# Kernel optimization log

Hardware: AMD Instinct MI355X
Metric: run time of the kernel (lower is better)

Reference implementation:

```python
import jax, jax.numpy as jnp
import numpy as np

# BatchNorm1d in eval mode with default init (gamma=1, beta=0, mean=0, var=1):
# y = x / sqrt(1 + eps)
BN_S = 1.0 / float(np.sqrt(1.0 + 1e-5))
ROI_THRESH = 0.8
DN = ('NCHW', 'OIHW', 'NCHW')


def conv(x, w, stride=1, pad=1):
    return jax.lax.conv_general_dilated(x, w, (stride, stride), ((pad, pad), (pad, pad)), dimension_numbers=DN)


def inv_conv(x, w):
    # dense equivalent of spconv.SparseInverseConv2d paired with a stride-2, pad-1, k=3 conv:
    # adjoint index map = transposed conv (lhs_dilation=2, flipped kernel, pad (1,2))
    return jax.lax.conv_general_dilated(x, jnp.flip(w, (2, 3)), (1, 1), ((1, 2), (1, 2)), lhs_dilation=(2, 2), dimension_numbers=DN)


def downsample_mask(m):
    # active-site generation rule of a stride-2, pad-1, k=3 sparse conv == 3x3/stride-2 max pool
    return jax.lax.reduce_window(m, 0.0, jax.lax.max, (1, 1, 3, 3), (1, 1, 2, 2), ((0, 0), (0, 0), (1, 1), (1, 1)))


def setup_inputs():
    key = jax.random.key(0)
    ks = jax.random.split(key, 24)
    b, n_i, H, W = 2, 4, 384, 384
    s = 0.1  # weight scale to keep activations bounded through the conv stack
    inp = {
        'x': jax.random.normal(ks[0], (b, 64, H // 4, W // 4), jnp.float32),
        'image': jax.random.normal(ks[1], (b, 3, H, W), jnp.float32),
        'masks': jax.random.uniform(ks[2], (b, n_i, H, W), jnp.float32),
        'roi_masks': jax.random.uniform(ks[3], (b, n_i, H, W), jnp.float32),
        'w1a': jax.random.normal(ks[4], (32, 4, 3, 3), jnp.float32) * s,
        'w1b': jax.random.normal(ks[5], (32, 32, 3, 3), jnp.float32) * s,
        'w2a': jax.random.normal(ks[6], (32, 32, 3, 3), jnp.float32) * s,
        'w2b': jax.random.normal(ks[7], (32, 32, 3, 3), jnp.float32) * s,
        'w4a': jax.random.normal(ks[8], (64, 32, 3, 3), jnp.float32) * s,
        'w4b': jax.random.normal(ks[9], (64, 64, 3, 3), jnp.float32) * s,
        'inv4_w': jax.random.normal(ks[10], (64, 64, 3, 3), jnp.float32) * s,
        'l4_sub_w': jax.random.normal(ks[11], (32, 64, 3, 3), jnp.float32) * s,
        'inv2_w': jax.random.normal(ks[12], (32, 32, 3, 3), jnp.float32) * s,
        'l5_sub_w': jax.random.normal(ks[13], (32, 32, 3, 3), jnp.float32) * s,
        'r4_w1': jax.random.normal(ks[14], (32, 64, 3, 3), jnp.float32) * s,
        'r4_w2': jax.random.normal(ks[15], (1, 32, 3, 3), jnp.float32) * s,
        'r4_b2': jax.random.normal(ks[16], (1,), jnp.float32) * s,
        'r1_w1': jax.random.normal(ks[17], (32, 32, 3, 3), jnp.float32) * s,
        'r1_w2': jax.random.normal(ks[18], (1, 32, 3, 3), jnp.float32) * s,
        'r1_b2': jax.random.normal(ks[19], (1,), jnp.float32) * s,
    }
    return inp


def reference(x, image, masks, roi_masks, w1a, w1b, w2a, w2b, w4a, w4b, inv4_w, l4_sub_w, inv2_w, l5_sub_w, r4_w1, r4_w2, r4_b2, r1_w1, r1_w2, r1_b2):
    # Faithful dense emulation of predict_details: SubMConv == conv(masked x)*mask,
    # stride-2 SparseConv == conv(masked x) masked by max-pooled mask,
    # SparseInverseConv == transposed conv masked by parent-resolution mask,
    # Fsp.sparse_add on shared indices == masked add, dense()-99/+99 == where(mask, v, -99).
    b, n_i, H, W = masks.shape
    N = b * n_i
    m = masks.reshape(N, 1, H, W)
    roi = roi_masks.reshape(N, 1, H, W)
    img = jnp.broadcast_to(image[:, None], (b, n_i, 3, H, W)).reshape(N, 3, H, W)
    inp = jnp.concatenate([img, m], axis=1)  # [N,4,H,W]

    mask1 = (roi > ROI_THRESH).astype(inp.dtype)
    mask2 = downsample_mask(mask1)
    mask4 = downsample_mask(mask2)

    # low_os1_module: SubMConv, ReLU, BN, SubMConv, ReLU, BN
    f = jnp.maximum(conv(inp * mask1, w1a) * mask1, 0.0) * BN_S
    fea1 = jnp.maximum(conv(f, w1b) * mask1, 0.0) * BN_S  # [N,32,H,W]
    # low_os2_module: stride-2 SparseConv, ReLU, BN, SubMConv, ReLU, BN
    g = jnp.maximum(conv(fea1, w2a, stride=2) * mask2, 0.0) * BN_S
    fea2 = jnp.maximum(conv(g, w2b) * mask2, 0.0) * BN_S  # [N,32,H/2,W/2]
    # low_os4_module
    h = jnp.maximum(conv(fea2, w4a, stride=2) * mask4, 0.0) * BN_S
    fea3 = jnp.maximum(conv(h, w4b) * mask4, 0.0) * BN_S  # [N,64,H/4,W/4]

    # gather dense OS4 features at sparse sites (batch index // n_i) + sparse_add
    xg = jnp.broadcast_to(x[:, None], (b, n_i) + x.shape[1:]).reshape(N, *x.shape[1:]) * mask4
    xs = xg + fea3

    # refine_OS4: SubMConv, BN, leaky, SubMConv(+bias); dense() with -99 off-support
    t = jax.nn.leaky_relu(conv(xs, r4_w1) * mask4 * BN_S, 0.2)
    t = (conv(t, r4_w2) + r4_b2[None, :, None, None]) * mask4
    x_os4_out = jnp.where(mask4 > 0, t, -99.0)

    # layer4: SparseInverseConv(64->64) to OS2 sites, BN, leaky, SubMConv(64->32); add fea2
    u = jax.nn.leaky_relu(inv_conv(xs, inv4_w) * mask2 * BN_S, 0.2)
    u = conv(u, l4_sub_w) * mask2 + fea2
    # layer5: SparseInverseConv(32->32) to OS1 sites, BN, leaky, SubMConv(32->32); add fea1
    v = jax.nn.leaky_relu(inv_conv(u, inv2_w) * mask1 * BN_S, 0.2)
    v = conv(v, l5_sub_w) * mask1 + fea1

    # refine_OS1
    t1 = jax.nn.leaky_relu(conv(v, r1_w1) * mask1 * BN_S, 0.2)
    t1 = (conv(t1, r1_w2) + r1_b2[None, :, None, None]) * mask1
    x_os1_out = jnp.where(mask1 > 0, t1, -99.0)
    return x_os4_out, x_os1_out
```

## Files before the change

kernel.cpp:

```cpp
#include <hip/hip_runtime.h>
#include <hip/hip_bf16.h>

using bf16 = __hip_bfloat16;
typedef unsigned char u8;
typedef short bf16x8 __attribute__((ext_vector_type(8)));
typedef short bf16x4 __attribute__((ext_vector_type(4)));
typedef float f32x4 __attribute__((ext_vector_type(4)));

#define BNS 0.9999950000374997f
#define MFMA_B16 __builtin_amdgcn_mfma_f32_16x16x32_bf16

__device__ __forceinline__ short f2bs(float v){ bf16 h = __float2bfloat16(v); return *reinterpret_cast<short*>(&h); }
__device__ __forceinline__ float s2f(short s){ union{unsigned u; float f;} x; x.u = ((unsigned)(unsigned short)s) << 16; return x.f; }
__device__ __forceinline__ float lrelu(float a){ return fmaxf(a, 0.2f*a); }
__device__ __forceinline__ bf16x8 ld8(const short* p){ return *(const bf16x8*)(p); }

__global__ __launch_bounds__(256) void k_prep(const float* __restrict__ roi,
                                              const float* __restrict__ w1b,
                                              const float* __restrict__ i2,
                                              const float* __restrict__ l5,
                                              const float* __restrict__ r1a,
                                              const float* __restrict__ w2b,
                                              const float* __restrict__ w2a,
                                              const float* __restrict__ inv4,
                                              const float* __restrict__ w4b,
                                              const float* __restrict__ l4s,
                                              const float* __restrict__ r4w1,
                                              const float* __restrict__ w4a,
                                              const float* __restrict__ w1a,
                                              const float* __restrict__ r1w2,
                                              const float* __restrict__ r4w2,
                                              u8* __restrict__ M1, u8* __restrict__ M2, u8* __restrict__ M4,
                                              short* __restrict__ WT, short* __restrict__ WT4,
                                              short* __restrict__ d1a, short* __restrict__ dh)
{
    const int HW1 = 384*384, HW2 = 192*192, HW4 = 96*96;
    int bid = blockIdx.x, tid = threadIdx.x;
    if (bid < 4608){
        int i = bid*256 + tid;
        M1[i] = (roi[i] > 0.8f) ? 1 : 0;
    } else if (bid < 5760){
        int i = (bid-4608)*256 + tid;
        int n = i / HW2, p = i - n*HW2;
        int oy = p / 192, ox = p - oy*192;
        const float* r = roi + (size_t)n*HW1;
        int v = 0;
        #pragma unroll
        for (int ky=0; ky<3; ky++){
            int iy = 2*oy + ky - 1;
            if ((unsigned)iy >= 384u) continue;
            #pragma unroll
            for (int kx=0; kx<3; kx++){
                int ix = 2*ox + kx - 1;
                if ((unsigned)ix < 384u) v |= (r[iy*384 + ix] > 0.8f);
            }
        }
        M2[i] = (u8)v;
    } else if (bid < 6048){
        int i = (bid-5760)*256 + tid;
        int n = i / HW4, p = i - n*HW4;
        int oy = p / 96, ox = p - oy*96;
        const float* r = roi + (size_t)n*HW1;
        int v = 0;
        for (int dy=-3; dy<=3; dy++){
            int iy = 4*oy + dy;
            if ((unsigned)iy >= 384u) continue;
            for (int dx=-3; dx<=3; dx++){
                int ix = 4*ox + dx;
                if ((unsigned)ix < 384u) v |= (r[iy*384 + ix] > 0.8f);
            }
        }
        M4[i] = (u8)v;
    } else if (bid < 6264){
        int local = bid - 6048;
        int a = local / 36;
        int j = (local - a*36)*256 + tid;
        const float* src = (a==0)? w1b : (a==1)? i2 : (a==2)? l5 : (a==3)? r1a : (a==4)? w2b : w2a;
        float sc = (a==2) ? 1.0f : BNS;
        if (j < 9216){
            int co = j/288, r = j%288, ci = r/9, k = r%9;
            WT[a*9216 + k*1024 + co*32 + ci] = f2bs(src[j]*sc);
        }
    } else if (bid < 6984){
        int local = bid - 6264;
        int a = local / 144;
        int j = (local - a*144)*256 + tid;
        if (a < 2){
            if (j < 36864){
                int co = j/576, r = j%576, ci = r/9, k = r%9;
                const float* s = a ? w4b : inv4;
                WT4[a*36864 + k*4096 + co*64 + ci] = f2bs(s[j]*BNS);
            }
        } else if (a < 4){
            if (j < 18432){
                int co = j/576, r = j%576, ci = r/9, k = r%9;
                const float* s = (a==2) ? l4s : r4w1;
                float sc = (a==2) ? 1.0f : BNS;
                WT4[73728 + (a-2)*18432 + k*2048 + co*64 + ci] = f2bs(s[j]*sc);
            }
        } else {
            if (j < 18432){
                int co = j/288, r = j%288, ci = r/9, k = r%9;
                WT4[110592 + k*2048 + co*32 + ci] = f2bs(w4a[j]*BNS);
            }
        }
    } else {
        int local = bid - 6984;
        int a = local / 18;
        int j = (local - a*18)*256 + tid;
        if (a == 0){
            if (j < 2048){
                int h = j >> 10, r = j & 1023, co = r >> 5, kq = r & 31;
                int q = h*32 + kq;
                d1a[j] = (q < 36) ? f2bs(w1a[co*36 + q]*BNS) : 0;
            }
        } else {
            if (j < 4608){
                int k = j/512, r = j%512, co = r/32, ci = r%32;
                const float* s = (a==1) ? r1w2 : r4w2;
                dh[(a-1)*4608 + j] = (co == 0) ? f2bs(s[ci*9 + k]) : 0;
            }
        }
    }
}

template<int CIN, int COUT, int EPI, int TH>
__global__ __launch_bounds__(256) void mconv_s1(const short* __restrict__ in, int H,
                                                const short* __restrict__ wT,
                                                const u8* __restrict__ mask,
                                                const float* __restrict__ res32,
                                                short* __restrict__ out, int tilesX)
{
    const int HW = H*H;
    const int HV = CIN/32, G = COUT/16, CH8 = CIN/8;
    const int SR = TH + 2;
    const int SITES = SR*18;
    const int PS = (SITES | 1)*8;
    const int U2N = TH/4;
    int tY = blockIdx.x / tilesX, tX = blockIdx.x % tilesX, n = blockIdx.z;
    int y0 = tY*TH, x0 = tX*16;

    __shared__ __align__(16) short s_in[CH8*((SITES|1)*8)];
    __shared__ u8 s_m[TH*16];

    int tid = threadIdx.x;
    const short* inN = in + (size_t)n*HW*CIN;
    for (int i = tid; i < SITES*CH8; i += 256){
        int r = i/CH8, q = i%CH8;
        int ry = r/18, rx = r%18;
        int gy = y0-1+ry, gx = x0-1+rx;
        bf16x8 v = {0,0,0,0,0,0,0,0};
        if ((unsigned)gy < (unsigned)H && (unsigned)gx < (unsigned)H)
            v = *(const bf16x8*)(inN + ((size_t)gy*H + gx)*CIN + q*8);
        *(bf16x8*)(s_in + q*PS + r*8) = v;
    }
    for (int i = tid; i < TH*16; i += 256){
        int ty = i>>4, tx = i&15;
        s_m[i] = mask[(size_t)n*HW + (y0+ty)*H + x0+tx];
    }
    __syncthreads();

    int wv = tid >> 6, lane = tid & 63;
    int nQ = lane >> 4, nn = lane & 15;

    f32x4 acc[U2N][G];
    #pragma unroll
    for (int u2=0; u2<U2N; ++u2)
        #pragma unroll
        for (int g=0; g<G; ++g) acc[u2][g] = (f32x4){0,0,0,0};

    #pragma unroll
    for (int h=0; h<HV; ++h){
        const short* bh[U2N];
        #pragma unroll
        for (int u2=0; u2<U2N; ++u2){
            int ty = u2*4 + wv;
            bh[u2] = s_in + (h*4+nQ)*PS + (ty*18 + nn)*8;
        }
        #pragma unroll
        for (int ky=0; ky<3; ++ky)
            #pragma unroll
            for (int kx=0; kx<3; ++kx){
                const int k = ky*3+kx;
                bf16x8 a[G];
                #pragma unroll
                for (int g=0; g<G; ++g)
                    a[g] = *(const bf16x8*)(wT + k*COUT*CIN + (g*16+nn)*CIN + h*32 + nQ*8);
                #pragma unroll
                for (int u2=0; u2<U2N; ++u2){
                    bf16x8 bfr = ld8(bh[u2] + (ky*18+kx)*8);
                    #pragma unroll
                    for (int g=0; g<G; ++g)
                        acc[u2][g] = MFMA_B16(a[g], bfr, acc[u2][g], 0,0,0);
                }
            }
    }

    #pragma unroll
    for (int u2=0; u2<U2N; ++u2){
        int nt = u2*4 + wv;
        int p = (y0+nt)*H + x0+nn;
        u8 m = s_m[nt*16 + nn];
        short* op = out + ((size_t)n*HW + p)*COUT;
        #pragma unroll
        for (int g=0; g<G; ++g){
            float r[4];
            #pragma unroll
            for (int e=0; e<4; ++e){
                int co = g*16 + nQ*4 + e;
                float a = acc[u2][g][e], o;
                if      (EPI == 0) o = m ? fmaxf(a,0.f) : 0.f;
                else if (EPI == 1) o = m ? lrelu(a) : 0.f;
                else o = m ? fmaxf(a,0.f) + res32[((size_t)(n>>2)*COUT + co)*(size_t)HW + p] : 0.f;
                r[e] = o;
            }
            bf16x4 w4 = {f2bs(r[0]),f2bs(r[1]),f2bs(r[2]),f2bs(r[3])};
            *(bf16x4*)(op + g*16 + nQ*4) = w4;
        }
    }
}

template<int COUT, int THO>
__global__ __launch_bounds__(256) void mconv_s2m(const short* __restrict__ in, int IH,
                                                 const short* __restrict__ wT,
                                                 const u8* __restrict__ mask,
                                                 short* __restrict__ out, int OH, int tilesX)
{
    const int IHW = IH*IH, OHW = OH*OH, G = COUT/16;
    const int IR = 2*THO + 1;
    const int SITES = IR*33;
    const int PS = (SITES|1)*8;
    const int ITN = THO/4;
    int tY = blockIdx.x / tilesX, tX = blockIdx.x % tilesX, n = blockIdx.z;
    int y0 = tY*THO, x0 = tX*16;

    __shared__ __align__(16) short s_in[4*((SITES|1)*8)];
    __shared__ u8 s_m[THO*16];

    int tid = threadIdx.x;
    const short* inN = in + (size_t)n*IHW*32;
    for (int i = tid; i < SITES*4; i += 256){
        int r = i>>2, q = i&3;
        int ry = r/33, rx = r%33;
        int gy = 2*y0-1+ry, gx = 2*x0-1+rx;
        bf16x8 v = {0,0,0,0,0,0,0,0};
        if ((unsigned)gy < (unsigned)IH && (unsigned)gx < (unsigned)IH)
            v = *(const bf16x8*)(inN + ((size_t)gy*IH + gx)*32 + q*8);
        *(bf16x8*)(s_in + q*PS + r*8) = v;
    }
    for (int i = tid; i < THO*16; i += 256){
        int ty = i>>4, tx = i&15;
        s_m[i] = mask[(size_t)n*OHW + (y0+ty)*OH + x0+tx];
    }
    __syncthreads();

    int wv = tid >> 6, lane = tid & 63;
    int nQ = lane >> 4, nn = lane & 15;

    f32x4 acc[ITN][G];
    #pragma unroll
    for (int it=0; it<ITN; ++it)
        #pragma unroll
        for (int g=0; g<G; ++g) acc[it][g] = (f32x4){0,0,0,0};

    const short* pb[ITN];
    #pragma unroll
    for (int it=0; it<ITN; ++it){
        int nt = it*4 + wv;
        pb[it] = s_in + nQ*PS + ((2*nt)*33 + 2*nn)*8;
    }

    #pragma unroll
    for (int ky=0; ky<3; ++ky)
        #pragma unroll
        for (int kx=0; kx<3; ++kx){
            const int k = ky*3+kx;
            bf16x8 a[G];
            #pragma unroll
            for (int g=0; g<G; ++g)
                a[g] = *(const bf16x8*)(wT + k*COUT*32 + (g*16+nn)*32 + nQ*8);
            #pragma unroll
            for (int it=0; it<ITN; ++it){
                bf16x8 bfr = ld8(pb[it] + (ky*33+kx)*8);
                #pragma unroll
                for (int g=0; g<G; ++g)
                    acc[it][g] = MFMA_B16(a[g], bfr, acc[it][g], 0,0,0);
            }
        }

    #pragma unroll
    for (int it=0; it<ITN; ++it){
        int nt = it*4 + wv;
        int p = (y0+nt)*OH + x0+nn;
        u8 m = s_m[nt*16 + nn];
        short* op = out + ((size_t)n*OHW + p)*COUT;
        #pragma unroll
        for (int g=0; g<G; ++g){
            float r[4];
            #pragma unroll
            for (int e=0; e<4; ++e) r[e] = m ? fmaxf(acc[it][g][e],0.f) : 0.f;
            bf16x4 w4 = {f2bs(r[0]),f2bs(r[1]),f2bs(r[2]),f2bs(r[3])};
            *(bf16x4*)(op + g*16 + nQ*4) = w4;
        }
    }
}

template<int TH>
__global__ __launch_bounds__(256) void mconv_ref4(const short* __restrict__ in, int H,
                                                  const short* __restrict__ wTa,
                                                  const short* __restrict__ wTh,
                                                  const float* __restrict__ bias,
                                                  const u8* __restrict__ mask,
                                                  float* __restrict__ out, int tilesX)
{
    const int HW = H*H;
    const int XR = TH+4, XSITES = XR*20;
    const int PSX = (XSITES|1)*8;
    const int TR = TH+2, TSITES = TR*18;
    const int PST = (TSITES|1)*8;
    int tY = blockIdx.x / tilesX, tX = blockIdx.x % tilesX, n = blockIdx.z;
    int y0 = tY*TH, x0 = tX*16;

    __shared__ __align__(16) short s_xs[8*((XSITES|1)*8)];
    __shared__ __align__(16) short s_t[4*((TSITES|1)*8)];
    __shared__ u8 s_m[TSITES];

    int tid = threadIdx.x;
    const short* inN = in + (size_t)n*HW*64;
    for (int i = tid; i < XSITES*8; i += 256){
        int r = i>>3, q = i&7;
        int ry = r/20, rx = r%20;
        int gy = y0-2+ry, gx = x0-2+rx;
        bf16x8 v = {0,0,0,0,0,0,0,0};
        if ((unsigned)gy < (unsigned)H && (unsigned)gx < (unsigned)H)
            v = *(const bf16x8*)(inN + ((size_t)gy*H + gx)*64 + q*8);
        *(bf16x8*)(s_xs + q*PSX + r*8) = v;
    }
    for (int i = tid; i < TSITES; i += 256){
        int vy = i/18, vx = i%18;
        int gy = y0-1+vy, gx = x0-1+vx;
        s_m[i] = ((unsigned)gy < (unsigned)H && (unsigned)gx < (unsigned)H) ? mask[(size_t)n*HW + gy*H + gx] : 0;
    }
    __syncthreads();

    int wv = tid >> 6, lane = tid & 63;
    int nQ = lane >> 4, nn = lane & 15;

    const int TG = (TSITES + 15)/16;
    for (int g8 = wv; g8 < TG; g8 += 4){
        int s0 = g8*16 + nn;
        int s = s0 >= TSITES ? TSITES-1 : s0;
        int vy = s/18, vx = s - vy*18;
        const short* pb = s_xs + nQ*PSX + (vy*20 + vx)*8;
        f32x4 acc0 = {0,0,0,0}, acc1 = {0,0,0,0};
        #pragma unroll
        for (int ky=0; ky<3; ++ky)
            #pragma unroll
            for (int kx=0; kx<3; ++kx){
                const int k = ky*3+kx;
                const short* wk = wTa + k*2048;
                bf16x8 xlo = ld8(pb + (ky*20+kx)*8);
                bf16x8 xhi = ld8(pb + 4*PSX + (ky*20+kx)*8);
                bf16x8 a0lo = *(const bf16x8*)(wk + nn*64 + nQ*8);
                bf16x8 a0hi = *(const bf16x8*)(wk + nn*64 + 32 + nQ*8);
                bf16x8 a1lo = *(const bf16x8*)(wk + (16+nn)*64 + nQ*8);
                bf16x8 a1hi = *(const bf16x8*)(wk + (16+nn)*64 + 32 + nQ*8);
                acc0 = MFMA_B16(a0lo, xlo, acc0, 0,0,0);
                acc0 = MFMA_B16(a0hi, xhi, acc0, 0,0,0);
                acc1 = MFMA_B16(a1lo, xlo, acc1, 0,0,0);
                acc1 = MFMA_B16(a1hi, xhi, acc1, 0,0,0);
            }
        if (s0 < TSITES){
            u8 m = s_m[s0];
            #pragma unroll
            for (int g=0; g<2; ++g){
                float r[4];
                #pragma unroll
                for (int e=0; e<4; ++e){
                    float a = g ? acc1[e] : acc0[e];
                    r[e] = m ? lrelu(a) : 0.f;
                }
                bf16x4 w4 = {f2bs(r[0]),f2bs(r[1]),f2bs(r[2]),f2bs(r[3])};
                *(bf16x4*)(s_t + (g*2 + (nQ>>1))*PST + s0*8 + (nQ&1)*4) = w4;
            }
        }
    }
    __syncthreads();

    float bb = bias[0];
    for (int nt = wv; nt < TH; nt += 4){
        const short* pt = s_t + nQ*PST + (nt*18 + nn)*8;
        f32x4 acc = {0,0,0,0};
        #pragma unroll
        for (int ky=0; ky<3; ++ky)
            #pragma unroll
            for (int kx=0; kx<3; ++kx){
                const int k = ky*3+kx;
                bf16x8 aw = *(const bf16x8*)(wTh + k*512 + nn*32 + nQ*8);
                bf16x8 bfr = ld8(pt + (ky*18+kx)*8);
                acc = MFMA_B16(aw, bfr, acc, 0,0,0);
            }
        if (nQ == 0){
            u8 m = s_m[(nt+1)*18 + nn+1];
            out[(size_t)n*HW + (size_t)(y0+nt)*H + (x0+nn)] = m ? acc[0] + bb : -99.f;
        }
    }
}

__global__ __launch_bounds__(256) void conv1ab3(const float* __restrict__ image,
                                                const float* __restrict__ masks,
                                                const u8*  __restrict__ M1,
                                                const short* __restrict__ wT1a,
                                                const short* __restrict__ wT1b,
                                                short* __restrict__ fea1)
{
    const int H = 384; const int HW = H*H;
    const int PS = 181*8;
    int tY = blockIdx.x / 48, tX = blockIdx.x % 48, n = blockIdx.z;
    int y0 = tY*16, x0 = tX*8;

    __shared__ float s_inp[4][240];
    __shared__ u8    s_m[240];
    __shared__ int   s_cnt[2];
    __shared__ unsigned short s_lF[180];
    __shared__ unsigned short s_lO[128];
    __shared__ __align__(16) short s_ic[8*(181*8)];
    __shared__ __align__(16) short s_f[4*(181*8)];

    int tid = threadIdx.x;
    const bf16x8 Z8 = {0,0,0,0,0,0,0,0};
    if (tid < 2) s_cnt[tid] = 0;
    for (int i = tid; i < 4*181; i += 256)
        *(bf16x8*)(s_f + i*8) = Z8;
    for (int i = tid; i < 240; i += 256){
        int ly = i/12, lxx = i%12;
        int gy = y0-2+ly, gx = x0-2+lxx;
        bool inb = ((unsigned)gy < 384u) && ((unsigned)gx < 384u);
        u8 mv = inb ? M1[(size_t)n*HW + gy*H + gx] : 0;
        s_m[i] = mv;
        float mm = (float)mv;
        int p = gy*H + gx;
        #pragma unroll
        for (int c = 0; c < 4; ++c){
            float v = 0.f;
            if (inb) v = (c < 3) ? image[((size_t)(n>>2)*3 + c)*HW + p]
                                 : masks[(size_t)n*HW + p];
            s_inp[c][i] = v*mm;
        }
    }
    __syncthreads();

    for (int i = tid; i < 180; i += 256){
        int fy = i/10, fx = i - fy*10;
        if (s_m[(fy+1)*12 + fx+1]){
            int idx = atomicAdd(&s_cnt[0], 1);
            s_lF[idx] = (unsigned short)i;
        }
    }
    for (int i = tid; i < 128; i += 256){
        int ty = i>>3, tx = i&7;
        if (s_m[(ty+2)*12 + tx+2]){
            int idx = atomicAdd(&s_cnt[1], 1);
            s_lO[idx] = (unsigned short)i;
        }
    }
    __syncthreads();

    int cntF = s_cnt[0], cntO = s_cnt[1];

    {
        int q = tid & 63;
        int ci = q/9, kk = q - ci*9, ky = kk/3, kx = kk - ky*3;
        bool qok = q < 36;
        for (int i = tid; i < cntF*64; i += 256){
            int site = s_lF[i >> 6];
            short v = 0;
            if (qok){
                int fy = site/10, fx = site - fy*10;
                v = f2bs(s_inp[ci][(fy+ky)*12 + fx+kx]);
            }
            s_ic[(q>>3)*PS + site*8 + (q&7)] = v;
        }
    }
    __syncthreads();

    int wv = tid >> 6, lane = tid & 63;
    int nQ = lane >> 4, nn = lane & 15;

    {
        bf16x8 fa0[2], fa1[2];
        #pragma unroll
        for (int h=0;h<2;++h){
            fa0[h] = *(const bf16x8*)(wT1a + h*1024 + nn*32 + nQ*8);
            fa1[h] = *(const bf16x8*)(wT1a + h*1024 + (16+nn)*32 + nQ*8);
        }
        for (int base = wv*16; base < cntF; base += 64){
            int slot = base + nn;
            bool on = slot < cntF;
            int site = s_lF[on ? slot : 0];
            f32x4 a0 = {0,0,0,0}, a1 = {0,0,0,0};
            #pragma unroll
            for (int h=0;h<2;++h){
                bf16x8 bfr = ld8(s_ic + (h*4+nQ)*PS + site*8);
                a0 = MFMA_B16(fa0[h], bfr, a0, 0,0,0);
                a1 = MFMA_B16(fa1[h], bfr, a1, 0,0,0);
            }
            if (on){
                #pragma unroll
                for (int g=0; g<2; ++g){
                    float r[4];
                    #pragma unroll
                    for (int e=0; e<4; ++e){
                        float a = g ? a1[e] : a0[e];
                        r[e] = fmaxf(a,0.f);
                    }
                    bf16x4 w4 = {f2bs(r[0]),f2bs(r[1]),f2bs(r[2]),f2bs(r[3])};
                    *(bf16x4*)(s_f + (g*2 + (nQ>>1))*PS + site*8 + (nQ&1)*4) = w4;
                }
            }
        }
    }
    __syncthreads();

    {
        for (int base = wv*16; base < cntO; base += 64){
            int slot = base + nn;
            bool on = slot < cntO;
            int os = s_lO[on ? slot : 0];
            int ty = os >> 3, tx = os & 7;
            const short* pb = s_f + nQ*PS + (ty*10 + tx)*8;
            f32x4 acc0 = {0,0,0,0}, acc1 = {0,0,0,0};
            #pragma unroll
            for (int ky=0; ky<3; ++ky)
                #pragma unroll
                for (int kx=0; kx<3; ++kx){
                    const int k = ky*3+kx;
                    bf16x8 a0 = *(const bf16x8*)(wT1b + k*1024 + nn*32 + nQ*8);
                    bf16x8 a1 = *(const bf16x8*)(wT1b + k*1024 + (16+nn)*32 + nQ*8);
                    bf16x8 bfr = ld8(pb + (ky*10+kx)*8);
                    acc0 = MFMA_B16(a0, bfr, acc0, 0,0,0);
                    acc1 = MFMA_B16(a1, bfr, acc1, 0,0,0);
                }
            if (on){
                short* fp = fea1 + ((size_t)n*HW + (size_t)(y0+ty)*H + (x0+tx))*32;
                #pragma unroll
                for (int g=0; g<2; ++g){
                    float r[4];
                    #pragma unroll
                    for (int e=0; e<4; ++e){
                        float a = g ? acc1[e] : acc0[e];
                        r[e] = fmaxf(a,0.f);
                    }
                    bf16x4 w4 = {f2bs(r[0]),f2bs(r[1]),f2bs(r[2]),f2bs(r[3])};
                    *(bf16x4*)(fp + g*16 + nQ*4) = w4;
                }
            }
        }
        for (int i = tid; i < 128*4; i += 256){
            int os = i >> 2, q = i & 3;
            int ty = os >> 3, tx = os & 7;
            if (!s_m[(ty+2)*12 + tx+2])
                *(bf16x8*)(fea1 + ((size_t)n*HW + (size_t)(y0+ty)*H + (x0+tx))*32 + q*8) = Z8;
        }
    }
}

__global__ __launch_bounds__(256) void fk_l4c(const short* __restrict__ xs,
                                              const short* __restrict__ fea2,
                                              const u8*  __restrict__ M2,
                                              const short* __restrict__ wTi4,
                                              const short* __restrict__ wTl4,
                                              short* __restrict__ u_out)
{
    const int H2 = 192, HW2 = H2*H2, H4 = 96, HW4 = H4*H4;
    const int PSX = 101*8, PSU = 325*8;
    int tY = blockIdx.x / 12, tX = blockIdx.x % 12, n = blockIdx.z;
    int y0 = tY*16, x0 = tX*16;
    int uy0 = (y0>>1) - 1, ux0 = (x0>>1) - 1;

    __shared__ __align__(16) short s_xs[8*(101*8)];
    __shared__ __align__(16) short s_ul[8*(325*8)];
    __shared__ u8 s_m[324];

    int tid = threadIdx.x;
    const short* xN = xs + (size_t)n*HW4*64;
    for (int i = tid; i < 100*8; i += 256){
        int r = i>>3, q = i&7;
        int ly = r/10, lxx = r%10;
        int gy = uy0+ly, gx = ux0+lxx;
        bf16x8 v = {0,0,0,0,0,0,0,0};
        if ((unsigned)gy < 96u && (unsigned)gx < 96u)
            v = *(const bf16x8*)(xN + ((size_t)gy*H4 + gx)*64 + q*8);
        *(bf16x8*)(s_xs + q*PSX + r*8) = v;
    }
    for (int i = tid; i < 324; i += 256){
        int ry = i/18, rx = i%18; int gy = y0-1+ry, gx = x0-1+rx;
        s_m[i] = ((unsigned)gy < 192u && (unsigned)gx < 192u) ? M2[(size_t)n*HW2 + gy*H2 + gx] : 0;
    }

    int wv = tid >> 6, lane = tid & 63;
    int nQ = lane >> 4, nn = lane & 15;

    bf16x4 pf2v[4][2];
    {
        const short* f2N = fea2 + (size_t)n*HW2*32;
        #pragma unroll
        for (int u2=0; u2<4; ++u2){
            int nt = u2*4 + wv;
            int p = (y0+nt)*H2 + x0+nn;
            const short* fp = f2N + (size_t)p*32;
            pf2v[u2][0] = *(const bf16x4*)(fp + nQ*4);
            pf2v[u2][1] = *(const bf16x4*)(fp + 16 + nQ*4);
        }
    }
    __syncthreads();

    for (int ui = wv; ui < 24; ui += 4){
        int cls = ui/6, nt = ui%6;
        int pY = cls >> 1, pX = cls & 1;
        int s0 = nt*16 + nn;
        int s = s0 > 80 ? 80 : s0;
        int jr = s/9, jc = s%9;
        int ry = 2*jr + pY, rx = 2*jc + pX;

        int tiy[4], tix[4], twk[4]; int tapN;
        if (pY == 0){
            if (pX == 0){
                tiy[0]=jr;   tix[0]=jc;   twk[0]=8;
                tiy[1]=jr;   tix[1]=jc+1; twk[1]=6;
                tiy[2]=jr+1; tix[2]=jc;   twk[2]=2;
                tiy[3]=jr+1; tix[3]=jc+1; twk[3]=0; tapN=4;
            } else {
                tiy[0]=jr;   tix[0]=jc+1; twk[0]=7;
                tiy[1]=jr+1; tix[1]=jc+1; twk[1]=1; tapN=2;
            }
        } else {
            if (pX == 0){
                tiy[0]=jr+1; tix[0]=jc;   twk[0]=5;
                tiy[1]=jr+1; tix[1]=jc+1; twk[1]=3; tapN=2;
            } else {
                tiy[0]=jr+1; tix[0]=jc+1; twk[0]=4; tapN=1;
            }
        }

        f32x4 acc[4];
        #pragma unroll
        for (int g=0; g<4; ++g) acc[g] = (f32x4){0,0,0,0};
        for (int t = 0; t < tapN; ++t){
            int off = (tiy[t]*10 + tix[t])*8;
            bf16x8 xlo = ld8(s_xs + nQ*PSX + off);
            bf16x8 xhi = ld8(s_xs + (4+nQ)*PSX + off);
            const short* wk = wTi4 + twk[t]*4096;
            #pragma unroll
            for (int g=0; g<4; ++g){
                bf16x8 alo = *(const bf16x8*)(wk + (g*16+nn)*64 + nQ*8);
                bf16x8 ahi = *(const bf16x8*)(wk + (g*16+nn)*64 + 32 + nQ*8);
                acc[g] = MFMA_B16(alo, xlo, acc[g], 0,0,0);
                acc[g] = MFMA_B16(ahi, xhi, acc[g], 0,0,0);
            }
        }
        if (s0 <= 80){
            int sidx = ry*18 + rx;
            u8 m = s_m[sidx];
            #pragma unroll
            for (int g=0; g<4; ++g){
                float r[4];
                #pragma unroll
                for (int e=0; e<4; ++e){
                    float a = acc[g][e];
                    r[e] = m ? lrelu(a) : 0.f;
                }
                bf16x4 w4 = {f2bs(r[0]),f2bs(r[1]),f2bs(r[2]),f2bs(r[3])};
                *(bf16x4*)(s_ul + ((g>>1)*4 + (g&1)*2 + (nQ>>1))*PSU + sidx*8 + (nQ&1)*4) = w4;
            }
        }
    }
    __syncthreads();

    {
        f32x4 acc0[4], acc1[4];
        const short* pv[4];
        #pragma unroll
        for (int u2=0; u2<4; ++u2){
            acc0[u2] = (f32x4){0,0,0,0}; acc1[u2] = (f32x4){0,0,0,0};
            int nt = u2*4 + wv;
            pv[u2] = s_ul + nQ*PSU + (nt*18 + nn)*8;
        }
        #pragma unroll
        for (int ky=0; ky<3; ++ky)
            #pragma unroll
            for (int kx=0; kx<3; ++kx){
                int k = ky*3+kx;
                const short* wk = wTl4 + k*2048;
                bf16x8 a0lo = *(const bf16x8*)(wk + nn*64 + nQ*8);
                bf16x8 a0hi = *(const bf16x8*)(wk + nn*64 + 32 + nQ*8);
                bf16x8 a1lo = *(const bf16x8*)(wk + (16+nn)*64 + nQ*8);
                bf16x8 a1hi = *(const bf16x8*)(wk + (16+nn)*64 + 32 + nQ*8);
                #pragma unroll
                for (int u2=0; u2<4; ++u2){
                    bf16x8 vlo = ld8(pv[u2] + (ky*18+kx)*8);
                    bf16x8 vhi = ld8(pv[u2] + 4*PSU + (ky*18+kx)*8);
                    acc0[u2] = MFMA_B16(a0lo, vlo, acc0[u2], 0,0,0);
                    acc0[u2] = MFMA_B16(a0hi, vhi, acc0[u2], 0,0,0);
                    acc1[u2] = MFMA_B16(a1lo, vlo, acc1[u2], 0,0,0);
                    acc1[u2] = MFMA_B16(a1hi, vhi, acc1[u2], 0,0,0);
                }
            }
        #pragma unroll
        for (int u2 = 0; u2 < 4; ++u2){
            int nt = u2*4 + wv;
            int p = (y0+nt)*H2 + x0+nn;
            u8 m = s_m[(nt+1)*18 + nn+1];
            short* up = u_out + ((size_t)n*HW2 + p)*32;
            #pragma unroll
            for (int g=0; g<2; ++g){
                float r[4];
                #pragma unroll
                for (int e=0; e<4; ++e){
                    float a = g ? acc1[u2][e] : acc0[u2][e];
                    r[e] = m ? a + s2f(pf2v[u2][g][e]) : 0.f;
                }
                bf16x4 w4 = {f2bs(r[0]),f2bs(r[1]),f2bs(r[2]),f2bs(r[3])};
                *(bf16x4*)(up + g*16 + nQ*4) = w4;
            }
        }
    }
}

__global__ __launch_bounds__(256) void fk_back8(const short* __restrict__ u,
                                                const short* __restrict__ fea1,
                                                const u8*  __restrict__ M1,
                                                const short* __restrict__ wTi2,
                                                const short* __restrict__ wTl5,
                                                const short* __restrict__ wTr1a,
                                                const short* __restrict__ wTr1b,
                                                const float* __restrict__ r1_b2,
                                                float* __restrict__ out1)
{
    const int H1 = 384, HW1 = H1*H1, H2 = 192, HW2 = H2*H2;
    const int PS_U = 97*8, PS_A = 309*8, PS_B = 241*8, PS_C = 181*8;
    int tY = blockIdx.x / 48, tX = blockIdx.x % 48, n = blockIdx.z;
    int y0 = tY*16, x0 = tX*8;
    int uy0 = (y0>>1) - 2, ux0 = (x0>>1) - 2;

    __shared__ __align__(16) short sP0[4*(309*8)];
    __shared__ __align__(16) short sP1[4*(241*8)];
    __shared__ u8 s_m[308];
    __shared__ int s_cnt[7];
    __shared__ unsigned s_lA[4*80];
    __shared__ unsigned s_lB[240];
    __shared__ unsigned s_lC[180];
    __shared__ unsigned s_lD[128];
    short* s_u  = sP1;
    short* s_vl = sP0;
    short* s_v  = sP1;
    short* s_t1 = sP0;

    int tid = threadIdx.x;
    const bf16x8 Z8 = {0,0,0,0,0,0,0,0};

    if (tid < 7) s_cnt[tid] = 0;
    const short* uN = u + (size_t)n*HW2*32;
    for (int i = tid; i < 96*4; i += 256){
        int r = i>>2, q = i&3;
        int ly = r >> 3, lxx = r & 7;
        int gy = uy0+ly, gx = ux0+lxx;
        bf16x8 v = Z8;
        if ((unsigned)gy < 192u && (unsigned)gx < 192u)
            v = *(const bf16x8*)(uN + ((size_t)gy*H2 + gx)*32 + q*8);
        *(bf16x8*)(s_u + q*PS_U + r*8) = v;
    }
    for (int i = tid; i < 308; i += 256){
        int ry = i/14, rx = i%14; int gy = y0-3+ry, gx = x0-3+rx;
        s_m[i] = ((unsigned)gy < 384u && (unsigned)gx < 384u) ? M1[(size_t)n*HW1 + gy*H1 + gx] : 0;
    }
    for (int i = tid; i < 4*309; i += 256)
        *(bf16x8*)(s_vl + i*8) = Z8;
    __syncthreads();

    for (int i = tid; i < 308; i += 256){
        if (s_m[i]){
            int ry = i/14, rx = i - ry*14;
            int cls = ((ry&1)<<1) | (rx&1);
            int jr = ry>>1, jc = rx>>1;
            int idx = atomicAdd(&s_cnt[cls], 1);
            s_lA[cls*80 + idx] = ((unsigned)i<<16) | (unsigned)(jr*8+jc);
        }
    }
    for (int i = tid; i < 240; i += 256){
        int vy = i/12, vx = i - vy*12;
        if (s_m[(vy+1)*14 + vx+1]){
            int idx = atomicAdd(&s_cnt[4], 1);
            s_lB[idx] = ((unsigned)i<<16) | (unsigned)(vy*14+vx);
        }
    }
    for (int i = tid; i < 180; i += 256){
        int qy = i/10, qx = i - qy*10;
        if (s_m[(qy+2)*14 + qx+2]){
            int idx = atomicAdd(&s_cnt[5], 1);
            s_lC[idx] = ((unsigned)i<<16) | (unsigned)(qy*12+qx);
        }
    }
    for (int i = tid; i < 128; i += 256){
        int ty = i>>3, tx = i&7;
        if (s_m[(ty+3)*14 + tx+3]){
            int idx = atomicAdd(&s_cnt[6], 1);
            s_lD[idx] = ((unsigned)i<<16) | (unsigned)(ty*10+tx);
        } else {
            out1[(size_t)n*HW1 + (size_t)(y0+ty)*H1 + (x0+tx)] = -99.f;
        }
    }
    __syncthreads();

    int wv = tid >> 6, lane = tid & 63;
    int nQ = lane >> 4, nn = lane & 15;

    int cntB = s_cnt[4];
    bf16x4 pfB[4][2];
    #pragma unroll
    for (int it=0; it<4; ++it){
        int slot = wv*16 + it*64 + nn;
        if (slot < cntB){
            unsigned e = s_lB[slot];
            int wr = e >> 16;
            int vy = wr/12, vx = wr - vy*12;
            const short* f1 = fea1 + ((size_t)n*HW1 + (size_t)(y0-2+vy)*H1 + (x0-2+vx))*32;
            pfB[it][0] = *(const bf16x4*)(f1 + nQ*4);
            pfB[it][1] = *(const bf16x4*)(f1 + 16 + nQ*4);
        }
    }

    {
        const int tN_[4]   = {4,2,2,1};
        const int tOff[4][4] = {{0,1,8,9},{1,9,9,9},{8,9,9,9},{9,9,9,9}};
        const int tWk [4][4] = {{8,6,2,0},{7,1,1,1},{5,3,3,3},{4,4,4,4}};
        int cnt = s_cnt[wv];
        int tn = tN_[wv];
        for (int base = 0; base < cnt; base += 16){
            int slot = base + nn;
            bool on = slot < cnt;
            unsigned e = s_lA[wv*80 + (on ? slot : 0)];
            int rb = e & 0xffff;
            f32x4 acc0 = {0,0,0,0}, acc1 = {0,0,0,0};
            for (int t = 0; t < tn; ++t){
                bf16x8 bfr = ld8(s_u + nQ*PS_U + (rb + tOff[wv][t])*8);
                const short* wp = wTi2 + tWk[wv][t]*1024;
                bf16x8 a0 = *(const bf16x8*)(wp + nn*32 + nQ*8);
                bf16x8 a1 = *(const bf16x8*)(wp + (16+nn)*32 + nQ*8);
                acc0 = MFMA_B16(a0, bfr, acc0, 0,0,0);
                acc1 = MFMA_B16(a1, bfr, acc1, 0,0,0);
            }
            if (on){
                int sidx = e >> 16;
                float r[8];
                #pragma unroll
                for (int g=0; g<2; ++g)
                    #pragma unroll
                    for (int ee=0; ee<4; ++ee)
                        r[g*4+ee] = lrelu(g ? acc1[ee] : acc0[ee]);
                bf16x4 w0 = {f2bs(r[0]),f2bs(r[1]),f2bs(r[2]),f2bs(r[3])};
                bf16x4 w1 = {f2bs(r[4]),f2bs(r[5]),f2bs(r[6]),f2bs(r[7])};
                *(bf16x4*)(s_vl + (nQ>>1)*PS_A     + sidx*8 + (nQ&1)*4) = w0;
                *(bf16x4*)(s_vl + (2+(nQ>>1))*PS_A + sidx*8 + (nQ&1)*4) = w1;
            }
        }
    }
    __syncthreads();

    for (int i = tid; i < 4*241; i += 256)
        *(bf16x8*)(s_v + i*8) = Z8;
    __syncthreads();

    {
        #pragma unroll
        for (int it=0; it<4; ++it){
            int base = wv*16 + it*64;
            if (base < cntB){
                int slot = base + nn;
                bool on = slot < cntB;
                unsigned e = s_lB[on ? slot : 0];
                int rb = e & 0xffff;
                int wr = e >> 16;
                const short* pv = s_vl + nQ*PS_A + rb*8;
                f32x4 acc0 = {0,0,0,0}, acc1 = {0,0,0,0};
                #pragma unroll
                for (int ky=0; ky<3; ++ky)
                    #pragma unroll
                    for (int kx=0; kx<3; ++kx){
                        const int k = ky*3+kx;
                        bf16x8 wb0 = *(const bf16x8*)(wTl5 + k*1024 + nn*32 + nQ*8);
                        bf16x8 wb1 = *(const bf16x8*)(wTl5 + k*1024 + (16+nn)*32 + nQ*8);
                        bf16x8 bfr = ld8(pv + (ky*14+kx)*8);
                        acc0 = MFMA_B16(wb0, bfr, acc0, 0,0,0);
                        acc1 = MFMA_B16(wb1, bfr, acc1, 0,0,0);
                    }
                if (on){
                    float r[8];
                    #pragma unroll
                    for (int ee=0; ee<4; ++ee){
                        r[ee]   = acc0[ee] + s2f(pfB[it][0][ee]);
                        r[4+ee] = acc1[ee] + s2f(pfB[it][1][ee]);
                    }
                    bf16x4 w0 = {f2bs(r[0]),f2bs(r[1]),f2bs(r[2]),f2bs(r[3])};
                    bf16x4 w1 = {f2bs(r[4]),f2bs(r[5]),f2bs(r[6]),f2bs(r[7])};
                    *(bf16x4*)(s_v + (nQ>>1)*PS_B     + wr*8 + (nQ&1)*4) = w0;
                    *(bf16x4*)(s_v + (2+(nQ>>1))*PS_B + wr*8 + (nQ&1)*4) = w1;
                }
            }
        }
    }
    __syncthreads();

    for (int i = tid; i < 4*181; i += 256)
        *(bf16x8*)(s_t1 + i*8) = Z8;
    __syncthreads();

    {
        int cnt = s_cnt[5];
        for (int base = wv*16; base < cnt; base += 64){
            int slot = base + nn;
            bool on = slot < cnt;
            unsigned e = s_lC[on ? slot : 0];
            int rb = e & 0xffff;
            const short* pv = s_v + nQ*PS_B + rb*8;
            f32x4 acc0 = {0,0,0,0}, acc1 = {0,0,0,0};
            #pragma unroll
            for (int ky=0; ky<3; ++ky)
                #pragma unroll
                for (int kx=0; kx<3; ++kx){
                    const int k = ky*3+kx;
                    bf16x8 wc0 = *(const bf16x8*)(wTr1a + k*1024 + nn*32 + nQ*8);
                    bf16x8 wc1 = *(const bf16x8*)(wTr1a + k*1024 + (16+nn)*32 + nQ*8);
                    bf16x8 bfr = ld8(pv + (ky*12+kx)*8);
                    acc0 = MFMA_B16(wc0, bfr, acc0, 0,0,0);
                    acc1 = MFMA_B16(wc1, bfr, acc1, 0,0,0);
                }
            if (on){
                int wr = e >> 16;
                float r[8];
                #pragma unroll
                for (int g=0; g<2; ++g)
                    #pragma unroll
                    for (int ee=0; ee<4; ++ee)
                        r[g*4+ee] = lrelu(g ? acc1[ee] : acc0[ee]);
                bf16x4 w0 = {f2bs(r[0]),f2bs(r[1]),f2bs(r[2]),f2bs(r[3])};
                bf16x4 w1 = {f2bs(r[4]),f2bs(r[5]),f2bs(r[6]),f2bs(r[7])};
                *(bf16x4*)(s_t1 + (nQ>>1)*PS_C     + wr*8 + (nQ&1)*4) = w0;
                *(bf16x4*)(s_t1 + (2+(nQ>>1))*PS_C + wr*8 + (nQ&1)*4) = w1;
            }
        }
    }
    __syncthreads();

    {
        float bb = r1_b2[0];
        int cnt = s_cnt[6];
        for (int base = wv*16; base < cnt; base += 64){
            int slot = base + nn;
            bool on = slot < cnt;
            unsigned e = s_lD[on ? slot : 0];
            int rb = e & 0xffff;
            const short* pt = s_t1 + nQ*PS_C + rb*8;
            f32x4 acc = {0,0,0,0};
            #pragma unroll
            for (int ky=0; ky<3; ++ky)
                #pragma unroll
                for (int kx=0; kx<3; ++kx){
                    const int k = ky*3+kx;
                    bf16x8 aw = *(const bf16x8*)(wTr1b + k*512 + nn*32 + nQ*8);
                    bf16x8 bfr = ld8(pt + (ky*10+kx)*8);
                    acc = MFMA_B16(aw, bfr, acc, 0,0,0);
                }
            if (on && nQ == 0){
                int wr = e >> 16;
                int ty = wr >> 3, tx = wr & 7;
                out1[(size_t)n*HW1 + (size_t)(y0+ty)*H1 + (x0+tx)] = acc[0] + bb;
            }
        }
    }
}


extern "C" void kernel_launch(void* const* d_in, const int* in_sizes, int n_in,
                              void* d_out, int out_size, void* d_ws, size_t ws_size,
                              hipStream_t stream)
{
    const float* x      = (const float*)d_in[0];
    const float* image  = (const float*)d_in[1];
    const float* masks  = (const float*)d_in[2];
    const float* roi    = (const float*)d_in[3];
    const float* w1a    = (const float*)d_in[4];
    const float* w1b    = (const float*)d_in[5];
    const float* w2a    = (const float*)d_in[6];
    const float* w2b    = (const float*)d_in[7];
    const float* w4a    = (const float*)d_in[8];
    const float* w4b    = (const float*)d_in[9];
    const float* inv4_w = (const float*)d_in[10];
    const float* l4_sub = (const float*)d_in[11];
    const float* inv2_w = (const float*)d_in[12];
    const float* l5_sub = (const float*)d_in[13];
    const float* r4_w1  = (const float*)d_in[14];
    const float* r4_w2  = (const float*)d_in[15];
    const float* r4_b2  = (const float*)d_in[16];
    const float* r1_w1  = (const float*)d_in[17];
    const float* r1_w2  = (const float*)d_in[18];
    const float* r1_b2  = (const float*)d_in[19];
    float* out = (float*)d_out;

    const int N = 8;
    const int H1 = 384, HW1 = 384*384;
    const int H2 = 192, HW2 = 192*192;
    const int H4 = 96,  HW4 = 96*96;

    char* wsp = (char*)d_ws;
    size_t off = 0;
    auto alloc = [&](size_t bytes) -> char* {
        char* p = wsp + off;
        off += (bytes + 255) & ~(size_t)255;
        return p;
    };
    bf16* FEA1 = (bf16*)alloc((size_t)N*32*HW1*2);
    u8*   M1   = (u8*)alloc((size_t)N*HW1);
    u8*   M2   = (u8*)alloc((size_t)N*HW2);
    u8*   M4   = (u8*)alloc((size_t)N*HW4);
    bf16* FEA2 = (bf16*)alloc((size_t)N*32*HW2*2);
    bf16* XS   = (bf16*)alloc((size_t)N*64*HW4*2);
    bf16* GU   = (bf16*)alloc((size_t)N*32*HW2*2);
    bf16* HT   = (bf16*)alloc((size_t)N*64*HW4*2);
    short* WT   = (short*)alloc(6*9216*2);
    short* WT4  = (short*)alloc((size_t)129024*2);
    short* WT1a = (short*)alloc(2048*2);
    short* WTh  = (short*)alloc(2*4608*2);
    (void)ws_size; (void)in_sizes; (void)n_in; (void)out_size;

    short* wT1b  = WT;
    short* wTi2  = WT + 9216;
    short* wTl5  = WT + 2*9216;
    short* wTr1a = WT + 3*9216;
    short* wT2b  = WT + 4*9216;
    short* wT2a  = WT + 5*9216;
    short* wTi4  = WT4;
    short* wT4b  = WT4 + 36864;
    short* wTl4  = WT4 + 73728;
    short* wTr4a = WT4 + 92160;
    short* wT4a  = WT4 + 110592;
    short* wTr1b = WTh;
    short* wTr4b = WTh + 4608;

    dim3 blk(256);

    k_prep<<<dim3(7038), blk, 0, stream>>>(roi, w1b, inv2_w, l5_sub, r1_w1, w2b, w2a,
                                           inv4_w, w4b, l4_sub, r4_w1, w4a,
                                           w1a, r1_w2, r4_w2,
                                           M1, M2, M4, WT, WT4, WT1a, WTh);

    conv1ab3<<<dim3(1152, 1, N), blk, 0, stream>>>(image, masks, M1, WT1a, wT1b, (short*)FEA1);
    mconv_s2m<32,8><<<dim3(288, 1, N), blk, 0, stream>>>((const short*)FEA1, H1, wT2a, M2, (short*)GU, H2, 12);
    mconv_s1<32,32,0,8><<<dim3(288, 1, N), blk, 0, stream>>>((const short*)GU, H2, wT2b, M2, nullptr, (short*)FEA2, 12);
    mconv_s2m<64,4><<<dim3(144, 1, N), blk, 0, stream>>>((const short*)FEA2, H2, wT4a, M4, (short*)HT, H4, 6);
    mconv_s1<64,64,3,4><<<dim3(144, 1, N), blk, 0, stream>>>((const short*)HT, H4, wT4b, M4, x, (short*)XS, 6);

    mconv_ref4<4><<<dim3(144, 1, N), blk, 0, stream>>>((const short*)XS, H4, wTr4a, wTr4b, r4_b2, M4, out, 6);

    fk_l4c<<<dim3(144, 1, N), blk, 0, stream>>>((const short*)XS, (const short*)FEA2, M2,
                                                wTi4, wTl4, (short*)GU);

    fk_back8<<<dim3(1152, 1, N), blk, 0, stream>>>((const short*)GU, (const short*)FEA1, M1,
                                                   wTi2, wTl5, wTr1a, wTr1b, r1_b2,
                                                   out + (size_t)N*HW4);
}
```

Before: 522.2 us.

## Fuse OS4 stride-2 conv and submanifold conv into one kernel with halo recompute

Replaces the two separate OS4 launches (stride-2 masked conv writing HT, then the 64->64 submanifold conv adding x) with one kernel. Each block loads a FEA2 patch into LDS, computes the intermediate 64-channel activations for its 4x16 tile plus a one-pixel halo into shared memory, then runs the second conv and adds the gathered x. This removes the HT global round trip and one launch, at the cost of recomputing halo sites and using more LDS per block.

Result: slower. 539.5 us (+3.3%).

```diff
diff --git a/kernel.cpp b/kernel.cpp
--- a/kernel.cpp
+++ b/kernel.cpp
@@ -305,6 +305,118 @@
     }
 }
 
+__global__ __launch_bounds__(256) void mconv_os4(const short* __restrict__ fea2,
+                                                 const short* __restrict__ wTa,
+                                                 const short* __restrict__ wTb,
+                                                 const u8* __restrict__ M4,
+                                                 const float* __restrict__ x,
+                                                 short* __restrict__ xs_out)
+{
+    const int H2 = 192, HW2 = H2*H2, H4 = 96, HW4 = H4*H4;
+    const int PSI = 481*8, PSH = 109*8;
+    int tY = blockIdx.x / 6, tX = blockIdx.x % 6, n = blockIdx.z;
+    int y0 = tY*4, x0 = tX*16;
+
+    __shared__ __align__(16) short s_in[4*(481*8)];
+    __shared__ __align__(16) short s_h[8*(109*8)];
+    __shared__ u8 s_m[108];
+
+    int tid = threadIdx.x;
+    const short* f2N = fea2 + (size_t)n*HW2*32;
+    for (int i = tid; i < 481*4; i += 256){
+        int r = i>>2, q = i&3;
+        int ry = r/37, rx = r%37;
+        int gy = 2*y0-3+ry, gx = 2*x0-3+rx;
+        bf16x8 v = {0,0,0,0,0,0,0,0};
+        if ((unsigned)gy < 192u && (unsigned)gx < 192u)
+            v = *(const bf16x8*)(f2N + ((size_t)gy*H2 + gx)*32 + q*8);
+        *(bf16x8*)(s_in + q*PSI + r*8) = v;
+    }
+    for (int i = tid; i < 108; i += 256){
+        int ry = i/18, rx = i%18;
+        int gy = y0-1+ry, gx = x0-1+rx;
+        s_m[i] = ((unsigned)gy < 96u && (unsigned)gx < 96u) ? M4[(size_t)n*HW4 + gy*H4 + gx] : 0;
+    }
+    __syncthreads();
+
+    int wv = tid >> 6, lane = tid & 63;
+    int nQ = lane >> 4, nn = lane & 15;
+
+    for (int ui = wv; ui < 7; ui += 4){
+        int s0 = ui*16 + nn;
+        int s = s0 > 107 ? 107 : s0;
+        int hy = s/18, hx = s%18;
+        f32x4 acc[4];
+        #pragma unroll
+        for (int g=0; g<4; ++g) acc[g] = (f32x4){0,0,0,0};
+        #pragma unroll
+        for (int ky=0; ky<3; ++ky)
+            #pragma unroll
+            for (int kx=0; kx<3; ++kx){
+                const int k = ky*3+kx;
+                bf16x8 bfr = ld8(s_in + nQ*PSI + ((2*hy+ky)*37 + 2*hx+kx)*8);
+                #pragma unroll
+                for (int g=0; g<4; ++g){
+                    bf16x8 a = *(const bf16x8*)(wTa + k*2048 + (g*16+nn)*32 + nQ*8);
+                    acc[g] = MFMA_B16(a, bfr, acc[g], 0,0,0);
+                }
+            }
+        if (s0 < 108){
+            u8 m = s_m[s0];
+            #pragma unroll
+            for (int g=0; g<4; ++g){
+                float r[4];
+                #pragma unroll
+                for (int e=0; e<4; ++e) r[e] = m ? fmaxf(acc[g][e],0.f) : 0.f;
+                bf16x4 w4 = {f2bs(r[0]),f2bs(r[1]),f2bs(r[2]),f2bs(r[3])};
+                *(bf16x4*)(s_h + (g*2 + (nQ>>1))*PSH + s0*8 + (nQ&1)*4) = w4;
+            }
+        }
+    }
+    __syncthreads();
+
+    {
+        int s0 = wv*16 + nn;
+        int ty = s0 >> 4, tx = s0 & 15;
+        f32x4 acc[4];
+        #pragma unroll
+        for (int g=0; g<4; ++g) acc[g] = (f32x4){0,0,0,0};
+        #pragma unroll
+        for (int ky=0; ky<3; ++ky)
+            #pragma unroll
+            for (int kx=0; kx<3; ++kx){
+                const int k = ky*3+kx;
+                int off = ((ty+ky)*18 + tx+kx)*8;
+                bf16x8 vlo = ld8(s_h + nQ*PSH + off);
+                bf16x8 vhi = ld8(s_h + (4+nQ)*PSH + off);
+                const short* wk = wTb + k*4096;
+                #pragma unroll
+                for (int g=0; g<4; ++g){
+                    bf16x8 alo = *(const bf16x8*)(wk + (g*16+nn)*64 + nQ*8);
+                    bf16x8 ahi = *(const bf16x8*)(wk + (g*16+nn)*64 + 32 + nQ*8);
+                    acc[g] = MFMA_B16(alo, vlo, acc[g], 0,0,0);
+                    acc[g] = MFMA_B16(ahi, vhi, acc[g], 0,0,0);
+                }
+            }
+        int gy = y0+ty, gx = x0+tx;
+        int p = gy*H4 + gx;
+        u8 m = s_m[(ty+1)*18 + tx+1];
+        short* op = xs_out + ((size_t)n*HW4 + p)*64;
+        #pragma unroll
+        for (int g=0; g<4; ++g){
+            float r[4];
+            #pragma unroll
+            for (int e=0; e<4; ++e){
+                int co = g*16 + nQ*4 + e;
+                float a = acc[g][e];
+                r[e] = m ? fmaxf(a,0.f) + x[((size_t)(n>>2)*64 + co)*(size_t)HW4 + p] : 0.f;
+            }
+            bf16x4 w4 = {f2bs(r[0]),f2bs(r[1]),f2bs(r[2]),f2bs(r[3])};
+            *(bf16x4*)(op + g*16 + nQ*4) = w4;
+        }
+    }
+}
+
 template<int TH>
 __global__ __launch_bounds__(256) void mconv_ref4(const short* __restrict__ in, int H,
                                                   const short* __restrict__ wTa,
@@ -1031,7 +1143,7 @@
     short* WT4  = (short*)alloc((size_t)129024*2);
     short* WT1a = (short*)alloc(2048*2);
     short* WTh  = (short*)alloc(2*4608*2);
-    (void)ws_size; (void)in_sizes; (void)n_in; (void)out_size;
+    (void)ws_size; (void)in_sizes; (void)n_in; (void)out_size; (void)HT;
 
     short* wT1b  = WT;
     short* wTi2  = WT + 9216;
@@ -1057,8 +1169,8 @@
     conv1ab3<<<dim3(1152, 1, N), blk, 0, stream>>>(image, masks, M1, WT1a, wT1b, (short*)FEA1);
     mconv_s2m<32,8><<<dim3(288, 1, N), blk, 0, stream>>>((const short*)FEA1, H1, wT2a, M2, (short*)GU, H2, 12);
     mconv_s1<32,32,0,8><<<dim3(288, 1, N), blk, 0, stream>>>((const short*)GU, H2, wT2b, M2, nullptr, (short*)FEA2, 12);
-    mconv_s2m<64,4><<<dim3(144, 1, N), blk, 0, stream>>>((const short*)FEA2, H2, wT4a, M4, (short*)HT, H4, 6);
-    mconv_s1<64,64,3,4><<<dim3(144, 1, N), blk, 0, stream>>>((const short*)HT, H4, wT4b, M4, x, (short*)XS, 6);
+
+    mconv_os4<<<dim3(144, 1, N), blk, 0, stream>>>((const short*)FEA2, wT4a, wT4b, M4, x, (short*)XS);
 
     mconv_ref4<4><<<dim3(144, 1, N), blk, 0, stream>>>((const short*)XS, H4, wTr4a, wTr4b, r4_b2, M4, out, 6);
 
```
